# Kernel optimization log

Hardware: AMD Instinct MI355X
Metric: run time of the kernel (lower is better)

## Reference

```python
import jax, jax.numpy as jnp
import numpy as np

N, V, E = 65536, 2048, 1024
TEMPERATURE = 0.5
EPS = 1e-10
LOG_PARAM_Q = -2.995732273553991


def _l2_normalize(x, axis):
    # matches torch F.normalize(p=2): x / max(||x||, 1e-12)
    n = jnp.sqrt(jnp.sum(x * x, axis=axis, keepdims=True))
    return x / jnp.maximum(n, 1e-12)


def setup_inputs() -> dict:
    key = jax.random.key(0)
    k1, k2, k3 = jax.random.split(key, 3)
    z = jax.random.normal(k1, (N, E), dtype=jnp.float32)
    emb_weight = jax.random.normal(k2, (V, E), dtype=jnp.float32)
    U = jax.random.uniform(k3, (N, V), dtype=jnp.float32)
    return {"z": z, "emb_weight": emb_weight, "U": U}


def reference(z, emb_weight, U):
    kappa_q = jnp.exp(jnp.float32(LOG_PARAM_Q)) + jnp.float32(1.0)
    zn = _l2_normalize(z, axis=1)              # [N, E]
    emb = _l2_normalize(emb_weight, axis=1)    # [V, E]
    # logit = -distances = kappa_q * z @ emb.T
    logit = kappa_q * jnp.matmul(zn, emb.T)    # [N, V]
    # gumbel-softmax sample (training branch)
    g = -jnp.log(-jnp.log(U + EPS) + EPS)
    tokens = jax.nn.softmax((logit + g) / TEMPERATURE, axis=-1)  # [N, V]
    z_q = jnp.matmul(tokens, emb)              # [N, E]
    return (tokens, z_q)
```

## Files before the change

### kernel.cpp

```cpp
#include <hip/hip_runtime.h>
#include <hip/hip_bf16.h>
#include <stdint.h>

typedef short bf16x8 __attribute__((ext_vector_type(8)));
typedef float floatx4 __attribute__((ext_vector_type(4)));

#define N_ROWS 65536
#define V_DIM 2048
#define E_DIM 1024

__device__ __forceinline__ short f2bf(float x) {
  union { float f; uint32_t u; } c; c.f = x;
  uint32_t r = (c.u + 0x7FFFu + ((c.u >> 16) & 1u)) >> 16;
  return (short)(uint16_t)r;
}
__device__ __forceinline__ float bf16f(short b) {
  union { uint32_t u; float f; } c; c.u = ((uint32_t)(uint16_t)b) << 16;
  return c.f;
}
__device__ __forceinline__ uint32_t f2e4m3(float x) {
  union { float f; uint32_t u; } c; c.f = x;
  const uint32_t s = (c.u >> 24) & 0x80u;
  float ax = fabsf(x);
  uint32_t code;
  if (ax < 0.015625f) {
    code = (uint32_t)__float2int_rn(ax * 512.0f);
  } else {
    c.f = ax;
    uint32_t r = c.u + 0x7FFFFu + ((c.u >> 20) & 1u);
    code = (r >> 20) - (120u << 3);
    if (code > 0x7Eu) code = 0x7Eu;
  }
  return s | code;
}

__device__ __forceinline__ float wave_sum(float v) {
#pragma unroll
  for (int o = 32; o > 0; o >>= 1) v += __shfl_xor(v, o);
  return v;
}
__device__ __forceinline__ float wave_max(float v) {
#pragma unroll
  for (int o = 32; o > 0; o >>= 1) v = fmaxf(v, __shfl_xor(v, o));
  return v;
}

__device__ __forceinline__ void gll16(const void* g, void* l) {
  __builtin_amdgcn_global_load_lds(
      (const __attribute__((address_space(1))) void*)g,
      (__attribute__((address_space(3))) void*)l, 16, 0, 0);
}

template <int FAST>
__global__ __launch_bounds__(256) void k_norm_all(
    const float* __restrict__ Z, const float* __restrict__ W,
    short* __restrict__ zn, unsigned char* __restrict__ zn8,
    short* __restrict__ embn, short* __restrict__ embnT,
    unsigned char* __restrict__ embn8) {
  const int t = threadIdx.x;
  const int w = t >> 6, l = t & 63;
  if (blockIdx.x < V_DIM) {
    const int v = blockIdx.x;
    const float4 val = *(const float4*)&W[(size_t)v * E_DIM + t * 4];
    float ss = val.x * val.x + val.y * val.y + val.z * val.z + val.w * val.w;
    ss = wave_sum(ss);
    __shared__ float red[4];
    if (l == 0) red[w] = ss;
    __syncthreads();
    ss = red[0] + red[1] + red[2] + red[3];
    const float inv = 1.0f / fmaxf(sqrtf(ss), 1e-12f);
    short4 o;
    o.x = f2bf(val.x * inv);
    o.y = f2bf(val.y * inv);
    o.z = f2bf(val.z * inv);
    o.w = f2bf(val.w * inv);
    if (!FAST) *(short4*)&embn[(size_t)v * E_DIM + t * 4] = o;
    embnT[(size_t)(t * 4 + 0) * V_DIM + v] = o.x;
    embnT[(size_t)(t * 4 + 1) * V_DIM + v] = o.y;
    embnT[(size_t)(t * 4 + 2) * V_DIM + v] = o.z;
    embnT[(size_t)(t * 4 + 3) * V_DIM + v] = o.w;
    const uint32_t p = f2e4m3(val.x * inv) | (f2e4m3(val.y * inv) << 8) |
                       (f2e4m3(val.z * inv) << 16) | (f2e4m3(val.w * inv) << 24);
    *(uint32_t*)&embn8[(size_t)v * E_DIM + t * 4] = p;
  } else {
    const int row = (blockIdx.x - V_DIM) * 4 + w;
    const float* zr = Z + (size_t)row * E_DIM;
    float4 v[4];
    float ss = 0.f;
#pragma unroll
    for (int i = 0; i < 4; ++i) {
      v[i] = *(const float4*)&zr[(i * 64 + l) * 4];
      ss += v[i].x * v[i].x + v[i].y * v[i].y + v[i].z * v[i].z + v[i].w * v[i].w;
    }
    ss = wave_sum(ss);
    const float SCALE = 2.0f * (expf(-2.995732273553991f) + 1.0f);
    const float inv = SCALE / fmaxf(sqrtf(ss), 1e-12f);
    unsigned char* zo8 = zn8 + (size_t)row * E_DIM;
#pragma unroll
    for (int i = 0; i < 4; ++i) {
      if (!FAST) {
        short4 o;
        o.x = f2bf(v[i].x * inv);
        o.y = f2bf(v[i].y * inv);
        o.z = f2bf(v[i].z * inv);
        o.w = f2bf(v[i].w * inv);
        *(short4*)&zn[(size_t)row * E_DIM + (i * 64 + l) * 4] = o;
      }
      const uint32_t p = f2e4m3(v[i].x * inv) | (f2e4m3(v[i].y * inv) << 8) |
                         (f2e4m3(v[i].z * inv) << 16) | (f2e4m3(v[i].w * inv) << 24);
      *(uint32_t*)&zo8[(i * 64 + l) * 4] = p;
    }
  }
}

__global__ __launch_bounds__(512, 4) void k_gemm_f8(
    const unsigned char* __restrict__ A8, const unsigned char* __restrict__ B8,
    const float* __restrict__ U, short* __restrict__ Pb,
    float* __restrict__ partials, int cpx) {
  __shared__ __align__(16) char Sm[73728];
  const int tid = threadIdx.x;
  const int wv = tid >> 6, lane = tid & 63;
  const int lr = lane & 15, lh = lane >> 4;
  const int wr = wv >> 1, wc = wv & 1;
  const int d = blockIdx.x;
  const int L = (d & 7) * cpx + (d >> 3);
  const int by = L >> 4, bx = L & 15;
  const int m0 = by * 256, n0 = bx * 128;
  const int sg8 = (((tid & 3) ^ ((tid >> 2) & 3)) << 4);
  const unsigned char* gA = A8 + (size_t)(m0 + (tid >> 2)) * E_DIM + sg8;
  const unsigned char* gB = B8 + (size_t)(n0 + (tid >> 2)) * E_DIM + sg8;
  const int t3 = lr & 3;
  const int soff0 = ((((lh >> 1) + 0) ^ t3) << 4) + (lh & 1) * 8;
  const int soff1 = ((((lh >> 1) + 2) ^ t3) << 4) + (lh & 1) * 8;
  const int arow = (wr * 64 + lr) * 64;
  const int brow = (wc * 64 + lr) * 64;

#pragma unroll
  for (int t = 0; t < 2; ++t) {
    char* sa = Sm + t * 16384;
    char* sb = Sm + 49152 + t * 8192;
    gll16(gA + t * 64, sa + wv * 1024);
    gll16(gA + (size_t)128 * E_DIM + t * 64, sa + 8192 + wv * 1024);
    gll16(gB + t * 64, sb + wv * 1024);
  }
  asm volatile("s_waitcnt vmcnt(3)" ::: "memory");
  __builtin_amdgcn_s_barrier();
  __builtin_amdgcn_sched_barrier(0);

  floatx4 acc[4][4] = {};

#define DO_TILE(KT, CB, SN, STAGE, VMN)                                             \
  {                                                                                 \
    const char* Ab_ = Sm + (CB) * 16384;                                            \
    const char* Bb_ = Sm + 49152 + (CB) * 8192;                                     \
    char* An_ = Sm + (SN) * 16384;                                                  \
    char* Bn_ = Sm + 49152 + (SN) * 8192;                                           \
    const size_t kc_ = (size_t)((KT) + 2) * 64;                                     \
    long bfr[4], af[4];                                                             \
                \
    _Pragma("unroll")                                                               \
    for (int n = 0; n < 4; ++n) bfr[n] = *(const long*)(Bb_ + brow + n * 1024 + soff0); \
    _Pragma("unroll")                                                               \
    for (int i = 0; i < 4; ++i) af[i] = *(const long*)(Ab_ + arow + i * 1024 + soff0); \
    if (STAGE) {                                                                    \
      gll16(gA + kc_, An_ + wv * 1024);                                             \
      gll16(gA + (size_t)128 * E_DIM + kc_, An_ + 8192 + wv * 1024);                \
    }                                                                               \
    __builtin_amdgcn_s_barrier();                                                   \
    asm volatile("s_waitcnt lgkmcnt(0)" ::: "memory");                              \
    __builtin_amdgcn_sched_barrier(0);                                              \
    __builtin_amdgcn_s_setprio(1);                                                  \
    _Pragma("unroll")                                                               \
    for (int i = 0; i < 4; ++i) {                                                   \
      _Pragma("unroll")                                                             \
      for (int n = 0; n < 4; ++n)                                                   \
        acc[i][n] =                                                                 \
            __builtin_amdgcn_mfma_f32_16x16x32_fp8_fp8(af[i], bfr[n], acc[i][n], 0, 0, 0); \
    }                                                                               \
    __builtin_amdgcn_s_setprio(0);                                                  \
    __builtin_amdgcn_s_barrier();                                                   \
                           \
    _Pragma("unroll")                                                               \
    for (int n = 0; n < 4; ++n) bfr[n] = *(const long*)(Bb_ + brow + n * 1024 + soff1); \
    _Pragma("unroll")                                                               \
    for (int i = 0; i < 4; ++i) af[i] = *(const long*)(Ab_ + arow + i * 1024 + soff1); \
    if (STAGE) gll16(gB + kc_, Bn_ + wv * 1024);                                    \
    __builtin_amdgcn_s_barrier();                                                   \
    asm volatile("s_waitcnt lgkmcnt(0)" ::: "memory");                              \
    __builtin_amdgcn_sched_barrier(0);                                              \
    __builtin_amdgcn_s_setprio(1);                                                  \
    _Pragma("unroll")                                                               \
    for (int i = 0; i < 4; ++i) {                                                   \
      _Pragma("unroll")                                                             \
      for (int n = 0; n < 4; ++n)                                                   \
        acc[i][n] =                                                                 \
            __builtin_amdgcn_mfma_f32_16x16x32_fp8_fp8(af[i], bfr[n], acc[i][n], 0, 0, 0); \
    }                                                                               \
    __builtin_amdgcn_s_setprio(0);                                                  \
    asm volatile("s_waitcnt vmcnt(" #VMN ")" ::: "memory");                         \
    __builtin_amdgcn_s_barrier();                                                   \
    __builtin_amdgcn_sched_barrier(0);                                              \
  }

  for (int kt = 0; kt < 12; kt += 3) {
    DO_TILE(kt + 0, 0, 2, 1, 3);
    DO_TILE(kt + 1, 1, 0, 1, 3);
    DO_TILE(kt + 2, 2, 1, 1, 3);
  }
  DO_TILE(12, 0, 2, 1, 3);
  DO_TILE(13, 1, 0, 1, 3);
  DO_TILE(14, 2, 0, 0, 0);
  DO_TILE(15, 0, 0, 0, 0);
#undef DO_TILE

  const int gr0 = m0 + wr * 64 + lh * 4;
  const int gc0 = n0 + wc * 64 + lr;
  float rs[4][4] = {};
#pragma unroll
  for (int m = 0; m < 4; ++m)
#pragma unroll
    for (int n = 0; n < 4; ++n) {
      const int col = gc0 + n * 16;
#pragma unroll
      for (int j = 0; j < 4; ++j) {
        const int row = gr0 + m * 16 + j;
        const size_t idx = (size_t)row * V_DIM + col;
        const float u = U[idx];
        const float e = __expf(acc[m][n][j] - 2.f * __logf(-__logf(u + 1e-10f) + 1e-10f));
        const short eb = f2bf(e);
        Pb[idx] = eb;
        rs[m][j] += bf16f(eb);
      }
    }
#pragma unroll
  for (int m = 0; m < 4; ++m)
#pragma unroll
    for (int j = 0; j < 4; ++j) {
      float s = rs[m][j];
      s += __shfl_xor(s, 1); s += __shfl_xor(s, 2);
      s += __shfl_xor(s, 4); s += __shfl_xor(s, 8);
      if (lr == 0)
        partials[(size_t)(gr0 + m * 16 + j) * 32 + bx * 2 + wc] = s;
    }
}

template <int KDIM, int NBX>
__global__ __launch_bounds__(512, 2) void k_gemm8(
    const short* __restrict__ A, const short* __restrict__ B,
    const float* __restrict__ invsum, float* __restrict__ C,
    float* __restrict__ tokens, int cpx) {
  __shared__ __align__(16) short Sm[65536];
  const int NT = KDIM / 32;
  const int tid = threadIdx.x;
  const int wv = tid >> 6, lane = tid & 63;
  const int lr = lane & 15, lh = lane >> 4;
  const int wr = wv >> 2, wc = wv & 3;
  const int d = blockIdx.x;
  const int L = (d & 7) * cpx + (d >> 3);
  const int by = L / NBX, bx = L % NBX;
  const int m0 = by * 256, n0 = bx * 256;
  const int sg = (((lane & 3) ^ ((lane >> 2) & 3) ^ ((lane >> 4) & 3)) << 3);
  const int srow = wv * 16 + (lane >> 2);
  const short* gA = A + (size_t)(m0 + srow) * KDIM + sg;
  const short* gB = B + (size_t)(n0 + srow) * KDIM + sg;
  const int fslot = lh ^ ((lr ^ (lr >> 2)) & 3);
  const int aoff = wr * 8192 + lr * 64 + fslot * 16;
  const int boff = wc * 4096 + lr * 64 + fslot * 16;

  float inv0 = invsum[m0 + srow];
  float inv1 = invsum[m0 + 128 + srow];

#pragma unroll
  for (int t = 0; t < 2; ++t) {
#pragma unroll
    for (int q = 0; q < 2; ++q) {
      gll16(gA + (size_t)(q * 128) * KDIM + t * 32, Sm + t * 8192 + q * 4096 + wv * 512);
      gll16(gB + (size_t)(q * 128) * KDIM + t * 32, Sm + 32768 + t * 8192 + q * 4096 + wv * 512);
    }
  }
  asm volatile("s_waitcnt vmcnt(4)" ::: "memory");
  __builtin_amdgcn_s_barrier();
  __builtin_amdgcn_sched_barrier(0);

  floatx4 acc[8][4] = {};

#define DO_TILE(KT, STAGE, VMN, TOKW_)                                              \
  {                                                                                 \
    const int cb_ = (KT) & 3;                                                       \
    const char* Ab_ = (const char*)Sm + cb_ * 16384;                                \
    const char* Bb_ = (const char*)Sm + 65536 + cb_ * 16384;                        \
    short* An_ = Sm + (((KT) + 2) & 3) * 8192;                                      \
    short* Bn_ = Sm + 32768 + (((KT) + 2) & 3) * 8192;                              \
    const size_t kc_ = (size_t)((KT) + 2) * 32;                                     \
    bf16x8 bfr[4], af[4];                                                           \
    _Pragma("unroll")                                                               \
    for (int n = 0; n < 4; ++n) bfr[n] = *(const bf16x8*)(Bb_ + boff + n * 1024);   \
    _Pragma("unroll")                                                               \
    for (int i = 0; i < 4; ++i) af[i] = *(const bf16x8*)(Ab_ + aoff + i * 1024);    \
    if (STAGE) {                                                                    \
      gll16(gA + kc_, An_ + wv * 512);                                              \
      gll16(gA + (size_t)128 * KDIM + kc_, An_ + 4096 + wv * 512);                  \
    }                                                                               \
    __builtin_amdgcn_s_barrier();                                                   \
    asm volatile("s_waitcnt lgkmcnt(0)" ::: "memory");                              \
    __builtin_amdgcn_sched_barrier(0);                                              \
    __builtin_amdgcn_s_setprio(1);                                                  \
    _Pragma("unroll")                                                               \
    for (int i = 0; i < 4; ++i) {                                                   \
      _Pragma("unroll")                                                             \
      for (int n = 0; n < 4; ++n)                                                   \
        acc[i][n] =                                                                 \
            __builtin_amdgcn_mfma_f32_16x16x32_bf16(af[i], bfr[n], acc[i][n], 0, 0, 0); \
    }                                                                               \
    __builtin_amdgcn_s_setprio(0);                                                  \
    __builtin_amdgcn_s_barrier();                                                   \
    _Pragma("unroll")                                                               \
    for (int i = 0; i < 4; ++i)                                                     \
      af[i] = *(const bf16x8*)(Ab_ + aoff + 4096 + i * 1024);                       \
    if (STAGE) {                                                                    \
      gll16(gB + kc_, Bn_ + wv * 512);                                              \
      gll16(gB + (size_t)128 * KDIM + kc_, Bn_ + 4096 + wv * 512);                  \
    }                                                                               \
    __builtin_amdgcn_s_barrier();                                                   \
    asm volatile("s_waitcnt lgkmcnt(0)" ::: "memory");                              \
    __builtin_amdgcn_sched_barrier(0);                                              \
    __builtin_amdgcn_s_setprio(1);                                                  \
    _Pragma("unroll")                                                               \
    for (int i = 0; i < 4; ++i) {                                                   \
      _Pragma("unroll")                                                             \
      for (int n = 0; n < 4; ++n)                                                   \
        acc[4 + i][n] =                                                             \
            __builtin_amdgcn_mfma_f32_16x16x32_bf16(af[i], bfr[n], acc[4 + i][n], 0, 0, 0); \
    }                                                                               \
    __builtin_amdgcn_s_setprio(0);                                                  \
    if (TOKW_) {                                                                    \
      const short* myA_ = Sm + cb_ * 8192 + wv * 512 + lane * 8;                    \
      const bf16x8 v0_ = *(const bf16x8*)myA_;                                      \
      const bf16x8 v1_ = *(const bf16x8*)(myA_ + 4096);                             \
      const size_t c0_ = (size_t)(KT) * 32 + sg;                                    \
      float4 a_, b_;                                                                \
      a_.x = bf16f(v0_[0]) * inv0; a_.y = bf16f(v0_[1]) * inv0;                     \
      a_.z = bf16f(v0_[2]) * inv0; a_.w = bf16f(v0_[3]) * inv0;                     \
      b_.x = bf16f(v0_[4]) * inv0; b_.y = bf16f(v0_[5]) * inv0;                     \
      b_.z = bf16f(v0_[6]) * inv0; b_.w = bf16f(v0_[7]) * inv0;                     \
      *(float4*)&tokens[(size_t)(m0 + srow) * KDIM + c0_] = a_;                     \
      *(float4*)&tokens[(size_t)(m0 + srow) * KDIM + c0_ + 4] = b_;                 \
      a_.x = bf16f(v1_[0]) * inv1; a_.y = bf16f(v1_[1]) * inv1;                     \
      a_.z = bf16f(v1_[2]) * inv1; a_.w = bf16f(v1_[3]) * inv1;                     \
      b_.x = bf16f(v1_[4]) * inv1; b_.y = bf16f(v1_[5]) * inv1;                     \
      b_.z = bf16f(v1_[6]) * inv1; b_.w = bf16f(v1_[7]) * inv1;                     \
      *(float4*)&tokens[(size_t)(m0 + 128 + srow) * KDIM + c0_] = a_;               \
      *(float4*)&tokens[(size_t)(m0 + 128 + srow) * KDIM + c0_ + 4] = b_;           \
    }                                                                               \
    asm volatile("s_waitcnt vmcnt(" #VMN ")" ::: "memory");                         \
    __builtin_amdgcn_s_barrier();                                                   \
    __builtin_amdgcn_sched_barrier(0);                                              \
  }

  {
    const int s = bx * 16;
    int kt = 0;
    for (; kt < s; ++kt) DO_TILE(kt, 1, 4, 0);
    DO_TILE(kt, 1, 8, 1);
    ++kt;
    for (; kt < s + 16 && kt < NT - 2; ++kt) DO_TILE(kt, 1, 12, 1);
    if (kt == s + 16) {
      DO_TILE(kt, 1, 8, 0);
      ++kt;
    }
    for (; kt < NT - 2; ++kt) DO_TILE(kt, 1, 4, 0);
    DO_TILE(NT - 2, 0, 0, ((NT - 2) >> 4) == bx);
    DO_TILE(NT - 1, 0, 0, ((NT - 1) >> 4) == bx);
  }
#undef DO_TILE

  const int gr0 = m0 + wr * 128 + lh * 4;
  const int gc0 = n0 + wc * 64 + lr;
#pragma unroll
  for (int m = 0; m < 8; ++m)
#pragma unroll
    for (int j = 0; j < 4; ++j) {
      const int row = gr0 + m * 16 + j;
      const float s = invsum[row];
#pragma unroll
      for (int n = 0; n < 4; ++n)
        C[(size_t)row * E_DIM + gc0 + n * 16] = acc[m][n][j] * s;
    }
}

__global__ __launch_bounds__(256) void k_rowsum_inv(const float* __restrict__ partials,
                                                    float* __restrict__ invsum) {
  const int r = blockIdx.x * 256 + threadIdx.x;
  const float4* p = (const float4*)&partials[(size_t)r * 32];
  float s = 0.f;
#pragma unroll
  for (int i = 0; i < 8; ++i) { float4 v = p[i]; s += v.x + v.y + v.z + v.w; }
  invsum[r] = 1.f / s;
}

__global__ __launch_bounds__(256) void k_gemm_nt(const short* __restrict__ A,
                                                 const short* __restrict__ B,
                                                 float* __restrict__ C,
                                                 int lda, int ldb, int ldc, int K) {
  __shared__ __align__(16) short As[128][64];
  __shared__ __align__(16) short Bs[128][64];
  const int t = threadIdx.x;
  const int w = t >> 6, l = t & 63;
  const int lr = l & 15, lh = l >> 4;
  const int m0 = blockIdx.y * 128, n0 = blockIdx.x * 128;
  const int wm = (w >> 1) * 64, wn = (w & 1) * 64;
  floatx4 acc[4][4] = {};
  for (int k0 = 0; k0 < K; k0 += 64) {
    __syncthreads();
#pragma unroll
    for (int i = 0; i < 4; ++i) {
      const int c = i * 256 + t;
      const int r = c >> 3, c8 = (c & 7) * 8;
      *(bf16x8*)&As[r][c8] = *(const bf16x8*)&A[(size_t)(m0 + r) * lda + k0 + c8];
      *(bf16x8*)&Bs[r][c8] = *(const bf16x8*)&B[(size_t)(n0 + r) * ldb + k0 + c8];
    }
    __syncthreads();
#pragma unroll
    for (int kk = 0; kk < 64; kk += 32) {
      bf16x8 af[4], bfr[4];
#pragma unroll
      for (int m = 0; m < 4; ++m) af[m] = *(const bf16x8*)&As[wm + m * 16 + lr][kk + lh * 8];
#pragma unroll
      for (int n = 0; n < 4; ++n) bfr[n] = *(const bf16x8*)&Bs[wn + n * 16 + lr][kk + lh * 8];
#pragma unroll
      for (int m = 0; m < 4; ++m)
#pragma unroll
        for (int n = 0; n < 4; ++n)
          acc[m][n] = __builtin_amdgcn_mfma_f32_16x16x32_bf16(af[m], bfr[n], acc[m][n], 0, 0, 0);
    }
  }
#pragma unroll
  for (int m = 0; m < 4; ++m)
#pragma unroll
    for (int n = 0; n < 4; ++n) {
      const int col = n0 + wn + n * 16 + lr;
#pragma unroll
      for (int j = 0; j < 4; ++j)
        C[(size_t)(m0 + wm + m * 16 + lh * 4 + j) * ldc + col] = acc[m][n][j];
    }
}

__global__ __launch_bounds__(256) void k_gemm_nt_f32a(const float* __restrict__ A,
                                                      const short* __restrict__ B,
                                                      float* __restrict__ C,
                                                      int lda, int ldb, int ldc, int K) {
  __shared__ __align__(16) short As[128][64];
  __shared__ __align__(16) short Bs[128][64];
  const int t = threadIdx.x;
  const int w = t >> 6, l = t & 63;
  const int lr = l & 15, lh = l >> 4;
  const int m0 = blockIdx.y * 128, n0 = blockIdx.x * 128;
  const int wm = (w >> 1) * 64, wn = (w & 1) * 64;
  floatx4 acc[4][4] = {};
  for (int k0 = 0; k0 < K; k0 += 64) {
    __syncthreads();
#pragma unroll
    for (int i = 0; i < 4; ++i) {
      const int c = i * 256 + t;
      const int r = c >> 3, c8 = (c & 7) * 8;
      const float4 a0 = *(const float4*)&A[(size_t)(m0 + r) * lda + k0 + c8];
      const float4 a1 = *(const float4*)&A[(size_t)(m0 + r) * lda + k0 + c8 + 4];
      bf16x8 va;
      va[0] = f2bf(a0.x); va[1] = f2bf(a0.y); va[2] = f2bf(a0.z); va[3] = f2bf(a0.w);
      va[4] = f2bf(a1.x); va[5] = f2bf(a1.y); va[6] = f2bf(a1.z); va[7] = f2bf(a1.w);
      *(bf16x8*)&As[r][c8] = va;
      *(bf16x8*)&Bs[r][c8] = *(const bf16x8*)&B[(size_t)(n0 + r) * ldb + k0 + c8];
    }
    __syncthreads();
#pragma unroll
    for (int kk = 0; kk < 64; kk += 32) {
      bf16x8 af[4], bfr[4];
#pragma unroll
      for (int m = 0; m < 4; ++m) af[m] = *(const bf16x8*)&As[wm + m * 16 + lr][kk + lh * 8];
#pragma unroll
      for (int n = 0; n < 4; ++n) bfr[n] = *(const bf16x8*)&Bs[wn + n * 16 + lr][kk + lh * 8];
#pragma unroll
      for (int m = 0; m < 4; ++m)
#pragma unroll
        for (int n = 0; n < 4; ++n)
          acc[m][n] = __builtin_amdgcn_mfma_f32_16x16x32_bf16(af[m], bfr[n], acc[m][n], 0, 0, 0);
    }
  }
#pragma unroll
  for (int m = 0; m < 4; ++m)
#pragma unroll
    for (int n = 0; n < 4; ++n) {
      const int col = n0 + wn + n * 16 + lr;
#pragma unroll
      for (int j = 0; j < 4; ++j)
        C[(size_t)(m0 + wm + m * 16 + lh * 4 + j) * ldc + col] = acc[m][n][j];
    }
}

__global__ __launch_bounds__(256) void k_gumbel_softmax(float* __restrict__ S,
                                                        const float* __restrict__ U) {
  const int t = threadIdx.x;
  const int w = t >> 6, l = t & 63;
  const size_t base = (size_t)blockIdx.x * V_DIM + t * 8;
  const float4 s0 = *(const float4*)&S[base];
  const float4 s1 = *(const float4*)&S[base + 4];
  const float4 u0 = *(const float4*)&U[base];
  const float4 u1 = *(const float4*)&U[base + 4];
  float x[8];
  x[0] = s0.x - 2.f * __logf(-__logf(u0.x + 1e-10f) + 1e-10f);
  x[1] = s0.y - 2.f * __logf(-__logf(u0.y + 1e-10f) + 1e-10f);
  x[2] = s0.z - 2.f * __logf(-__logf(u0.z + 1e-10f) + 1e-10f);
  x[3] = s0.w - 2.f * __logf(-__logf(u0.w + 1e-10f) + 1e-10f);
  x[4] = s1.x - 2.f * __logf(-__logf(u1.x + 1e-10f) + 1e-10f);
  x[5] = s1.y - 2.f * __logf(-__logf(u1.y + 1e-10f) + 1e-10f);
  x[6] = s1.z - 2.f * __logf(-__logf(u1.z + 1e-10f) + 1e-10f);
  x[7] = s1.w - 2.f * __logf(-__logf(u1.w + 1e-10f) + 1e-10f);
  float lm = x[0];
#pragma unroll
  for (int i = 1; i < 8; ++i) lm = fmaxf(lm, x[i]);
  lm = wave_max(lm);
  __shared__ float redA[4], redB[4];
  if (l == 0) redA[w] = lm;
  __syncthreads();
  const float m = fmaxf(fmaxf(redA[0], redA[1]), fmaxf(redA[2], redA[3]));
  float p[8];
  float ls = 0.f;
#pragma unroll
  for (int i = 0; i < 8; ++i) { p[i] = __expf(x[i] - m); ls += p[i]; }
  ls = wave_sum(ls);
  if (l == 0) redB[w] = ls;
  __syncthreads();
  const float inv = 1.0f / (redB[0] + redB[1] + redB[2] + redB[3]);
  float4 o0 = make_float4(p[0] * inv, p[1] * inv, p[2] * inv, p[3] * inv);
  float4 o1 = make_float4(p[4] * inv, p[5] * inv, p[6] * inv, p[7] * inv);
  *(float4*)&S[base] = o0;
  *(float4*)&S[base + 4] = o1;
}

extern "C" void kernel_launch(void* const* d_in, const int* in_sizes, int n_in,
                              void* d_out, int out_size, void* d_ws, size_t ws_size,
                              hipStream_t stream) {
  const float* z = (const float*)d_in[0];
  const float* W = (const float*)d_in[1];
  const float* U = (const float*)d_in[2];
  float* tokens = (float*)d_out;
  float* zq = tokens + (size_t)N_ROWS * V_DIM;
  short* zn = (short*)zq;
  unsigned char* zn8 =
      (unsigned char*)zq + (size_t)N_ROWS * E_DIM * 2;

  short* embn = (short*)d_ws;
  short* embnT = embn + (size_t)V_DIM * E_DIM;
  unsigned char* embn8 = (unsigned char*)(embnT + (size_t)V_DIM * E_DIM);

  const size_t NEED = (size_t)V_DIM * E_DIM * 2 * 2
                    + (size_t)V_DIM * E_DIM
                    + (size_t)N_ROWS * 32 * 4
                    + (size_t)N_ROWS * 4
                    + (size_t)N_ROWS * V_DIM * 2;

  if (ws_size >= NEED) {
    float* partials = (float*)(embn8 + (size_t)V_DIM * E_DIM);
    float* invsum = partials + (size_t)N_ROWS * 32;
    short* Pb = (short*)(invsum + N_ROWS);
    k_norm_all<1><<<V_DIM + N_ROWS / 4, 256, 0, stream>>>(
        z, W, zn, zn8, embn, embnT, embn8);
    k_gemm_f8<<<4096, 512, 0, stream>>>(zn8, embn8, U, Pb, partials, 4096 / 8);
    k_rowsum_inv<<<N_ROWS / 256, 256, 0, stream>>>(partials, invsum);
    k_gemm8<V_DIM, 4><<<1024, 512, 0, stream>>>(
        Pb, embnT, invsum, zq, tokens, 1024 / 8);
  } else {
    k_norm_all<0><<<V_DIM + N_ROWS / 4, 256, 0, stream>>>(
        z, W, zn, zn8, embn, embnT, embn8);
    k_gemm_nt<<<dim3(V_DIM / 128, N_ROWS / 128), 256, 0, stream>>>(
        zn, embn, tokens, E_DIM, E_DIM, V_DIM, E_DIM);
    k_gumbel_softmax<<<N_ROWS, 256, 0, stream>>>(tokens, U);
    k_gemm_nt_f32a<<<dim3(E_DIM / 128, N_ROWS / 128), 256, 0, stream>>>(
        tokens, embnT, zq, V_DIM, V_DIM, E_DIM, V_DIM);
  }
}
```

Baseline: 846.1 us.

## Fuse row-sum inversion into second GEMM and prefetch U in epilogue

Removes the separate rowsum-inverse kernel; each block of the second GEMM now reduces the per-row partial sums into an LDS invsum array at kernel start. This cuts one launch and a global round-trip, at the cost of redundant partial reads per column block. The first GEMM's epilogue now loads U values one row-group ahead in double-buffered registers, overlapping global loads with the transcendental math. This raises register pressure.

```diff
diff --git a/kernel.cpp b/kernel.cpp
--- a/kernel.cpp
+++ b/kernel.cpp
@@ -157,7 +157,6 @@
     char* Bn_ = Sm + 49152 + (SN) * 8192;                                           \
     const size_t kc_ = (size_t)((KT) + 2) * 64;                                     \
     long bfr[4], af[4];                                                             \
-                \
     _Pragma("unroll")                                                               \
     for (int n = 0; n < 4; ++n) bfr[n] = *(const long*)(Bb_ + brow + n * 1024 + soff0); \
     _Pragma("unroll")                                                               \
@@ -179,7 +178,6 @@
     }                                                                               \
     __builtin_amdgcn_s_setprio(0);                                                  \
     __builtin_amdgcn_s_barrier();                                                   \
-                           \
     _Pragma("unroll")                                                               \
     for (int n = 0; n < 4; ++n) bfr[n] = *(const long*)(Bb_ + brow + n * 1024 + soff1); \
     _Pragma("unroll")                                                               \
@@ -216,22 +214,41 @@
   const int gr0 = m0 + wr * 64 + lh * 4;
   const int gc0 = n0 + wc * 64 + lr;
   float rs[4][4] = {};
-#pragma unroll
-  for (int m = 0; m < 4; ++m)
-#pragma unroll
-    for (int n = 0; n < 4; ++n) {
-      const int col = gc0 + n * 16;
-#pragma unroll
-      for (int j = 0; j < 4; ++j) {
-        const int row = gr0 + m * 16 + j;
-        const size_t idx = (size_t)row * V_DIM + col;
-        const float u = U[idx];
-        const float e = __expf(acc[m][n][j] - 2.f * __logf(-__logf(u + 1e-10f) + 1e-10f));
-        const short eb = f2bf(e);
-        Pb[idx] = eb;
-        rs[m][j] += bf16f(eb);
-      }
-    }
+  float ua[16], ub[16];
+
+#define U_LOAD(arr, m)                                                              \
+  _Pragma("unroll")                                                                 \
+  for (int n = 0; n < 4; ++n)                                                       \
+    _Pragma("unroll")                                                               \
+    for (int j = 0; j < 4; ++j)                                                     \
+      arr[n * 4 + j] = U[(size_t)(gr0 + (m) * 16 + j) * V_DIM + gc0 + n * 16];
+#define EPI_M(m, arr)                                                               \
+  _Pragma("unroll")                                                                 \
+  for (int n = 0; n < 4; ++n) {                                                     \
+    const int col = gc0 + n * 16;                                                   \
+    _Pragma("unroll")                                                               \
+    for (int j = 0; j < 4; ++j) {                                                   \
+      const int row = gr0 + (m) * 16 + j;                                           \
+      const size_t idx = (size_t)row * V_DIM + col;                                 \
+      const float e = __expf(acc[m][n][j] -                                         \
+                             2.f * __logf(-__logf(arr[n * 4 + j] + 1e-10f) + 1e-10f)); \
+      const short eb = f2bf(e);                                                     \
+      Pb[idx] = eb;                                                                 \
+      rs[m][j] += bf16f(eb);                                                        \
+    }                                                                               \
+  }
+
+  U_LOAD(ua, 0);
+  U_LOAD(ub, 1);
+  EPI_M(0, ua);
+  U_LOAD(ua, 2);
+  EPI_M(1, ub);
+  U_LOAD(ub, 3);
+  EPI_M(2, ua);
+  EPI_M(3, ub);
+#undef U_LOAD
+#undef EPI_M
+
 #pragma unroll
   for (int m = 0; m < 4; ++m)
 #pragma unroll
@@ -247,9 +264,10 @@
 template <int KDIM, int NBX>
 __global__ __launch_bounds__(512, 2) void k_gemm8(
     const short* __restrict__ A, const short* __restrict__ B,
-    const float* __restrict__ invsum, float* __restrict__ C,
+    const float* __restrict__ partials, float* __restrict__ C,
     float* __restrict__ tokens, int cpx) {
   __shared__ __align__(16) short Sm[65536];
+  __shared__ float invsum_lds[256];
   const int NT = KDIM / 32;
   const int tid = threadIdx.x;
   const int wv = tid >> 6, lane = tid & 63;
@@ -267,8 +285,18 @@
   const int aoff = wr * 8192 + lr * 64 + fslot * 16;
   const int boff = wc * 4096 + lr * 64 + fslot * 16;
 
-  float inv0 = invsum[m0 + srow];
-  float inv1 = invsum[m0 + 128 + srow];
+  {
+    const int r = tid >> 1;
+    const float4* p = (const float4*)&partials[(size_t)(m0 + r) * 32 + (tid & 1) * 16];
+    float s = 0.f;
+#pragma unroll
+    for (int i = 0; i < 4; ++i) { float4 v = p[i]; s += v.x + v.y + v.z + v.w; }
+    s += __shfl_xor(s, 1);
+    if ((tid & 1) == 0) invsum_lds[r] = 1.f / s;
+  }
+  __builtin_amdgcn_s_barrier();
+  const float inv0 = invsum_lds[srow];
+  const float inv1 = invsum_lds[128 + srow];
 
 #pragma unroll
   for (int t = 0; t < 2; ++t) {
@@ -381,21 +409,11 @@
 #pragma unroll
     for (int j = 0; j < 4; ++j) {
       const int row = gr0 + m * 16 + j;
-      const float s = invsum[row];
+      const float s = invsum_lds[row - m0];
 #pragma unroll
       for (int n = 0; n < 4; ++n)
         C[(size_t)row * E_DIM + gc0 + n * 16] = acc[m][n][j] * s;
     }
-}
-
-__global__ __launch_bounds__(256) void k_rowsum_inv(const float* __restrict__ partials,
-                                                    float* __restrict__ invsum) {
-  const int r = blockIdx.x * 256 + threadIdx.x;
-  const float4* p = (const float4*)&partials[(size_t)r * 32];
-  float s = 0.f;
-#pragma unroll
-  for (int i = 0; i < 8; ++i) { float4 v = p[i]; s += v.x + v.y + v.z + v.w; }
-  invsum[r] = 1.f / s;
 }
 
 __global__ __launch_bounds__(256) void k_gemm_nt(const short* __restrict__ A,
@@ -561,14 +579,13 @@
 
   if (ws_size >= NEED) {
     float* partials = (float*)(embn8 + (size_t)V_DIM * E_DIM);
-    float* invsum = partials + (size_t)N_ROWS * 32;
-    short* Pb = (short*)(invsum + N_ROWS);
+    float* spare = partials + (size_t)N_ROWS * 32;
+    short* Pb = (short*)(spare + N_ROWS);
     k_norm_all<1><<<V_DIM + N_ROWS / 4, 256, 0, stream>>>(
         z, W, zn, zn8, embn, embnT, embn8);
     k_gemm_f8<<<4096, 512, 0, stream>>>(zn8, embn8, U, Pb, partials, 4096 / 8);
-    k_rowsum_inv<<<N_ROWS / 256, 256, 0, stream>>>(partials, invsum);
     k_gemm8<V_DIM, 4><<<1024, 512, 0, stream>>>(
-        Pb, embnT, invsum, zq, tokens, 1024 / 8);
+        Pb, embnT, partials, zq, tokens, 1024 / 8);
   } else {
     k_norm_all<0><<<V_DIM + N_ROWS / 4, 256, 0, stream>>>(
         z, W, zn, zn8, embn, embnT, embn8);
```

Result: slower. 903.6 us (+6.8%).
